# Kernel optimization log

Hardware: AMD Instinct MI355X
Metric: run time of the kernel (lower is better)

Reference implementation:

```python
import jax, jax.numpy as jnp
import numpy as np

B, N, M, D = 2, 2048, 32, 128
H, DH = 8, 16
DI = H * DH            # dim_inner = 128
S = 5                  # 1 + max_degree + max_degree, max_degree = 2
DMLP = 256             # int(2.0 * dim_inner)


def _ln(x, g):  # LayerNorm(bias=False)
    mu = x.mean(-1, keepdims=True)
    var = ((x - mu) ** 2).mean(-1, keepdims=True)
    return (x - mu) / jnp.sqrt(var + 1e-5) * g


def _softclamp(t, v=50.0):
    return jnp.tanh(t / v) * v


def _gather(a, idx):  # a: [b, n, ...], idx: [b, i, j] -> [b, i, j, ...]
    return jax.vmap(lambda t, ix: jnp.take(t, ix, axis=0))(a, idx)


def setup_inputs():
    key = jax.random.key(0)
    ks = jax.random.split(key, 24)
    w = lambda k, i, o: jax.random.normal(k, (i, o), jnp.float32) / np.sqrt(i)
    return {
        'h': jax.random.normal(ks[0], (B, N, D), jnp.float32),
        't_ij': jax.random.normal(ks[1], (B, N, M, D), jnp.float32),
        'r_ij_1': jax.random.normal(ks[2], (B, N, M, 3), jnp.float32),
        'r_ij_2': jax.random.normal(ks[3], (B, N, M, 5), jnp.float32),
        'x_1': jax.random.normal(ks[4], (B, N, D, 3), jnp.float32),
        'x_2': jax.random.normal(ks[5], (B, N, D, 5), jnp.float32),
        'g_hi': jnp.ones((D,), jnp.float32),
        'g_hj': jnp.ones((D,), jnp.float32),
        'Wq': w(ks[6], D, DI),
        'Wk': w(ks[7], D, DI),
        'Wv1': w(ks[8], D, DMLP), 'bv1': jnp.zeros((DMLP,), jnp.float32),
        'Wv2': w(ks[9], DMLP, S * DI), 'bv2': jnp.zeros((S * DI,), jnp.float32),
        'Wp1': w(ks[10], D, DMLP), 'bp1': jnp.zeros((DMLP,), jnp.float32),
        'Wp2': w(ks[11], DMLP, S * DI), 'bp2': jnp.zeros((S * DI,), jnp.float32),
        'Wek': w(ks[12], D, S * DI),
        'Wev': w(ks[13], D, S * DI),
        'Wg': w(ks[14], D, H * S), 'bg': jnp.zeros((H * S,), jnp.float32),
        'Wc': w(ks[15], DI, D),
        'neighbor_indices': jax.random.randint(ks[16], (B, N, M), 0, N),
        'neighbor_mask': jnp.ones((B, N, M), bool),
    }


def reference(h, t_ij, r_ij_1, r_ij_2, x_1, x_2, g_hi, g_hj, Wq, Wk, Wv1, bv1,
              Wv2, bv2, Wp1, bp1, Wp2, bp2, Wek, Wev, Wg, bg, Wc,
              neighbor_indices, neighbor_mask):
    b, n, m = neighbor_indices.shape
    hi = _ln(h, g_hi)
    hj = _ln(h, g_hj)
    q = (hi @ Wq).reshape(b, n, H, DH).transpose(0, 2, 1, 3)               # b h i dh
    k = hj @ Wk                                                            # b n (h dh)
    v = jax.nn.silu(hj @ Wv1 + bv1) @ Wv2 + bv2                            # b n (s h dh)
    pav = jax.nn.silu(hj @ Wp1 + bp1) @ Wp2 + bp2                          # post-attn h values
    ek = jax.nn.silu(t_ij @ Wek)                                           # b i j (s h dh)
    ev = t_ij @ Wev
    # neighbor gathers over the node axis
    k_g = _gather(k, neighbor_indices)                                     # b i j (h dh)
    v_g = _gather(v, neighbor_indices)                                     # b i j (s h dh)
    pav_g = _gather(pav, neighbor_indices)
    heads4 = lambda t: t.reshape(b, n, m, H, DH).transpose(0, 3, 1, 2, 4)          # b h i j dh
    heads5 = lambda t: t.reshape(b, n, m, S, H, DH).transpose(0, 4, 1, 2, 3, 5)    # b h i j s dh
    keys = heads4(k_g)[..., None, :] * heads5(ek)                          # edge-fused keys
    sim = _softclamp(jnp.einsum('bhid,bhijsd->bhijs', q, keys))
    sim = jnp.where(neighbor_mask[:, None, :, :, None], sim, -jnp.finfo(sim.dtype).max)
    attn = jax.nn.softmax(sim, axis=-2)                                    # softmax over neighbors j
    sea = attn[..., None] * heads5(v_g) + heads5(ev) * heads5(pav_g)       # b h i j s dh
    gates = jax.nn.sigmoid(hi @ Wg + bg).reshape(b, n, H, S)               # layout (h s)
    sea = sea * gates.transpose(0, 2, 1, 3)[:, :, :, None, :, None]        # b h i 1 s 1
    out = sea.transpose(0, 2, 3, 4, 1, 5).reshape(b, n, m, S, DI) @ Wc     # b i j s d
    h_res = out[..., 0, :].sum(axis=2)                                     # sum over neighbors
    x_res = []
    for li, (r_l, x_l) in enumerate(((r_ij_1, x_1), (r_ij_2, x_2))):
        r_part = jnp.einsum('bijm,bijd->bidm', r_l, out[..., 1 + li, :])
        xg = _gather(x_l, neighbor_indices)                                # b i j d ml
        x_res.append(r_part + jnp.einsum('bijdm,bijd->bidm', xg, out[..., 3 + li, :]))
    return (h_res, x_res[0], x_res[1])
```

## Files before the change

### kernel.cpp

```cpp
#include <hip/hip_runtime.h>
#include <hip/hip_bf16.h>
#include <cstdint>


typedef __bf16 bf16x8 __attribute__((ext_vector_type(8)));
typedef float  f32x4  __attribute__((ext_vector_type(4)));
typedef unsigned short u16;
typedef unsigned int   u32;

__device__ __forceinline__ float sigm_(float x){ return 1.f/(1.f+__expf(-x)); }
__device__ __forceinline__ float silu_(float x){ return x/(1.f+__expf(-x)); }
__device__ __forceinline__ u16 f2b(float f){
    union{float f; u32 u;} x; x.f = f;
    u32 r = x.u + 0x7FFFu + ((x.u>>16)&1u);
    return (u16)(r>>16);
}
__device__ __forceinline__ float b2f(u16 b){
    union{u32 u; float f;} x; x.u = ((u32)b)<<16; return x.f;
}
union VecU { uint4 u; bf16x8 v; u16 s[8]; };
union Vec4 { uint2 u; u16 s[4]; };
__device__ __forceinline__ bf16x8 ld8(const u16* p){ VecU x; x.u = *(const uint4*)p; return x.v; }

__global__ __launch_bounds__(256) void prep_kernel(
    const float* __restrict__ Wek, const float* __restrict__ Wev,
    const float* __restrict__ Wc,
    const float* __restrict__ x1, const float* __restrict__ x2,
    u16* __restrict__ wekT, u16* __restrict__ wevT, u16* __restrict__ wcT,
    float* __restrict__ xT1, float* __restrict__ xT2, int do_xt)
{
    const int idx = blockIdx.x*256 + threadIdx.x;
    if (idx < 81920) {
        const int n = idx >> 7, k = idx & 127;
        wekT[idx] = f2b(Wek[k*640 + n]);
        wevT[idx] = f2b(Wev[k*640 + n]);
    }
    if (idx < 16384) {
        const int d = idx >> 7, c = idx & 127;
        wcT[idx] = f2b(Wc[c*128 + d]);
    }
    if (do_xt) {
        if (idx < 4096*384) {
            const int node = idx/384, rem = idx%384, m = rem>>7, d = rem&127;
            xT1[idx] = x1[((size_t)node*128 + d)*3 + m];
        }
        if (idx < 4096*640) {
            const int node = idx/640, rem = idx%640, m = rem>>7, d = rem&127;
            xT2[idx] = x2[((size_t)node*128 + d)*5 + m];
        }
    }
}

__global__ __launch_bounds__(256) void node_kernel(
    const float* __restrict__ h,
    const float* __restrict__ g_hi, const float* __restrict__ g_hj,
    const float* __restrict__ Wq, const float* __restrict__ Wk,
    const float* __restrict__ Wv1, const float* __restrict__ bv1,
    const float* __restrict__ Wv2, const float* __restrict__ bv2,
    const float* __restrict__ Wp1, const float* __restrict__ bp1,
    const float* __restrict__ Wp2, const float* __restrict__ bp2,
    const float* __restrict__ Wg, const float* __restrict__ bg,
    float* __restrict__ qws, float* __restrict__ kws,
    float* __restrict__ vws, float* __restrict__ pavws, float* __restrict__ gws)
{
    const int tid  = threadIdx.x;
    const int base = blockIdx.x * 8;
    __shared__ __align__(16) float hi_s[8][128];
    __shared__ __align__(16) float hj_s[8][128];
    __shared__ __align__(16) float u_s[8][256];

    {
        const int wv = tid >> 6, lane = tid & 63;
        for (int r = wv; r < 8; r += 4) {
            const int node = base + r;
            float a  = h[node*128 + lane];
            float b2 = h[node*128 + 64 + lane];
            float s = a + b2;
            #pragma unroll
            for (int off = 32; off > 0; off >>= 1) s += __shfl_down(s, off);
            s = __shfl(s, 0);
            const float mu = s * (1.f/128.f);
            const float da = a - mu, db = b2 - mu;
            float v = da*da + db*db;
            #pragma unroll
            for (int off = 32; off > 0; off >>= 1) v += __shfl_down(v, off);
            v = __shfl(v, 0);
            const float rstd = rsqrtf(v*(1.f/128.f) + 1e-5f);
            hi_s[r][lane]    = da*rstd*g_hi[lane];
            hi_s[r][64+lane] = db*rstd*g_hi[64+lane];
            hj_s[r][lane]    = da*rstd*g_hj[lane];
            hj_s[r][64+lane] = db*rstd*g_hj[64+lane];
        }
    }
    __syncthreads();

    {
        const int o  = tid & 127;
        const int r0 = (tid >> 7) * 4;
        float aq[4], ak[4];
        #pragma unroll
        for (int r=0;r<4;r++){ aq[r]=0.f; ak[r]=0.f; }
        for (int c0=0;c0<128;c0+=4) {
            float wq0=Wq[(c0+0)*128+o], wq1=Wq[(c0+1)*128+o], wq2=Wq[(c0+2)*128+o], wq3=Wq[(c0+3)*128+o];
            float wk0=Wk[(c0+0)*128+o], wk1=Wk[(c0+1)*128+o], wk2=Wk[(c0+2)*128+o], wk3=Wk[(c0+3)*128+o];
            #pragma unroll
            for (int r=0;r<4;r++) {
                float4 hi4 = *(const float4*)(&hi_s[r0+r][c0]);
                float4 hj4 = *(const float4*)(&hj_s[r0+r][c0]);
                aq[r] += hi4.x*wq0; aq[r] += hi4.y*wq1; aq[r] += hi4.z*wq2; aq[r] += hi4.w*wq3;
                ak[r] += hj4.x*wk0; ak[r] += hj4.y*wk1; ak[r] += hj4.z*wk2; ak[r] += hj4.w*wk3;
            }
        }
        #pragma unroll
        for (int r=0;r<4;r++) {
            qws[(size_t)(base+r0+r)*128 + o] = aq[r];
            kws[(size_t)(base+r0+r)*128 + o] = ak[r];
        }
    }

    {
        const int o = tid;
        float acc[8];
        const float bias = bv1[o];
        #pragma unroll
        for (int r=0;r<8;r++) acc[r]=bias;
        for (int c0=0;c0<128;c0+=4) {
            float w0=Wv1[(c0+0)*256+o], w1=Wv1[(c0+1)*256+o], w2=Wv1[(c0+2)*256+o], w3=Wv1[(c0+3)*256+o];
            #pragma unroll
            for (int r=0;r<8;r++) {
                float4 u4 = *(const float4*)(&hj_s[r][c0]);
                acc[r] += u4.x*w0; acc[r] += u4.y*w1; acc[r] += u4.z*w2; acc[r] += u4.w*w3;
            }
        }
        #pragma unroll
        for (int r=0;r<8;r++) u_s[r][o] = silu_(acc[r]);
    }
    __syncthreads();

    for (int o=tid; o<640; o+=256) {
        float acc[8];
        const float bias = bv2[o];
        #pragma unroll
        for (int r=0;r<8;r++) acc[r]=bias;
        for (int c0=0;c0<256;c0+=4) {
            float w0=Wv2[(c0+0)*640+o], w1=Wv2[(c0+1)*640+o], w2=Wv2[(c0+2)*640+o], w3=Wv2[(c0+3)*640+o];
            #pragma unroll
            for (int r=0;r<8;r++) {
                float4 u4 = *(const float4*)(&u_s[r][c0]);
                acc[r] += u4.x*w0; acc[r] += u4.y*w1; acc[r] += u4.z*w2; acc[r] += u4.w*w3;
            }
        }
        #pragma unroll
        for (int r=0;r<8;r++) vws[(size_t)(base+r)*640 + o] = acc[r];
    }
    __syncthreads();

    {
        const int o = tid;
        float acc[8];
        const float bias = bp1[o];
        #pragma unroll
        for (int r=0;r<8;r++) acc[r]=bias;
        for (int c0=0;c0<128;c0+=4) {
            float w0=Wp1[(c0+0)*256+o], w1=Wp1[(c0+1)*256+o], w2=Wp1[(c0+2)*256+o], w3=Wp1[(c0+3)*256+o];
            #pragma unroll
            for (int r=0;r<8;r++) {
                float4 u4 = *(const float4*)(&hj_s[r][c0]);
                acc[r] += u4.x*w0; acc[r] += u4.y*w1; acc[r] += u4.z*w2; acc[r] += u4.w*w3;
            }
        }
        #pragma unroll
        for (int r=0;r<8;r++) u_s[r][o] = silu_(acc[r]);
    }
    __syncthreads();

    for (int o=tid; o<640; o+=256) {
        float acc[8];
        const float bias = bp2[o];
        #pragma unroll
        for (int r=0;r<8;r++) acc[r]=bias;
        for (int c0=0;c0<256;c0+=4) {
            float w0=Wp2[(c0+0)*640+o], w1=Wp2[(c0+1)*640+o], w2=Wp2[(c0+2)*640+o], w3=Wp2[(c0+3)*640+o];
            #pragma unroll
            for (int r=0;r<8;r++) {
                float4 u4 = *(const float4*)(&u_s[r][c0]);
                acc[r] += u4.x*w0; acc[r] += u4.y*w1; acc[r] += u4.z*w2; acc[r] += u4.w*w3;
            }
        }
        #pragma unroll
        for (int r=0;r<8;r++) pavws[(size_t)(base+r)*640 + o] = acc[r];
    }

    for (int idx=tid; idx<8*40; idx+=256) {
        const int r = idx/40, hs = idx%40;
        float s = bg[hs];
        for (int c=0;c<128;c++) s += hi_s[r][c]*Wg[c*40+hs];
        gws[(size_t)(base+r)*40 + hs] = sigm_(s);
    }
}

template<bool XT>
__global__ __launch_bounds__(512,4) void edge_kernel(
    const float* __restrict__ t_ij,
    const float* __restrict__ r1, const float* __restrict__ r2,
    const float* __restrict__ x1, const float* __restrict__ x2,
    const float* __restrict__ xT1, const float* __restrict__ xT2,
    const u16* __restrict__ wekT, const u16* __restrict__ wevT,
    const u16* __restrict__ wcT,
    const int* __restrict__ nidx,
    const float* __restrict__ qws, const float* __restrict__ kws,
    const float* __restrict__ vws, const float* __restrict__ pavws,
    const float* __restrict__ gws,
    float* __restrict__ out)
{
    const int node = blockIdx.x;
    const int bN   = (node >> 11) << 11;
    const int tid  = threadIdx.x;
    const int grp  = tid >> 8;
    const int ltid = tid & 255;
    const int lane = ltid & 63, w = ltid >> 6;
    const int ll   = lane & 15, lh = lane >> 4;

    __shared__ __align__(16) u16   tj_s[32*128];
    __shared__ __align__(16) u16   chunk_s[2][80*128];
    __shared__ float sim_s[32][40];
    __shared__ __align__(16) float q_s[128];
    __shared__ float g_s[40];
    __shared__ int   jn_s[32];

    u16* chunk = chunk_s[grp];

    if (tid < 32) jn_s[tid] = nidx[node*32 + tid];
    else if (tid >= 64 && tid < 192) q_s[tid-64] = qws[(size_t)node*128 + (tid-64)];
    else if (tid >= 192 && tid < 232) g_s[tid-192] = gws[(size_t)node*40 + (tid-192)];
    __syncthreads();

    bf16x8 wcf[2][4];
    #pragma unroll
    for (int dlt=0;dlt<2;dlt++)
        #pragma unroll
        for (int ks=0;ks<4;ks++)
            wcf[dlt][ks] = ld8(wcT + (size_t)((w*2+dlt)*16 + ll)*128 + ks*32 + lh*8);

    float kq[16];
    if (ltid < 128) {
        const int j = grp*16 + (ltid >> 3), c0 = (ltid & 7) * 16;
        const float* tp = t_ij + (size_t)node*4096 + j*128 + c0;
        float4 t0 = *(const float4*)(tp+0);
        float4 t1 = *(const float4*)(tp+4);
        float4 t2 = *(const float4*)(tp+8);
        float4 t3 = *(const float4*)(tp+12);
        VecU p0, p1;
        p0.s[0]=f2b(t0.x); p0.s[1]=f2b(t0.y); p0.s[2]=f2b(t0.z); p0.s[3]=f2b(t0.w);
        p0.s[4]=f2b(t1.x); p0.s[5]=f2b(t1.y); p0.s[6]=f2b(t1.z); p0.s[7]=f2b(t1.w);
        p1.s[0]=f2b(t2.x); p1.s[1]=f2b(t2.y); p1.s[2]=f2b(t2.z); p1.s[3]=f2b(t2.w);
        p1.s[4]=f2b(t3.x); p1.s[5]=f2b(t3.y); p1.s[6]=f2b(t3.z); p1.s[7]=f2b(t3.w);
        const int el = (j*128 + c0) ^ ((j&7)<<3);
        *(uint4*)(tj_s + el)       = p0.u;
        *(uint4*)(tj_s + (el ^ 8)) = p1.u;

        const float* kp = kws + ((size_t)(bN + jn_s[j]))*128 + c0;
        #pragma unroll
        for (int i=0;i<16;i+=4) {
            float4 kv = *(const float4*)(kp+i);
            float4 qv = *(const float4*)(&q_s[c0+i]);
            kq[i+0] = qv.x*kv.x; kq[i+1] = qv.y*kv.y;
            kq[i+2] = qv.z*kv.z; kq[i+3] = qv.w*kv.w;
        }
    }
    __syncthreads();

    bf16x8 tfr[4];
    #pragma unroll
    for (int ks=0;ks<4;ks++) {
        const int j = grp*16 + ll;
        tfr[ks] = ld8(tj_s + ((j*128 + ks*32 + lh*8) ^ ((j&7)<<3)));
    }
    #pragma unroll 2
    for (int t=0;t<10;t++) {
        const int nt = w + 4*t;
        const u16* wp = wekT + (size_t)(nt*16 + ll)*128 + lh*8;
        __builtin_amdgcn_s_setprio(1);
        f32x4 aA = {0.f,0.f,0.f,0.f}, aB = {0.f,0.f,0.f,0.f};
        aA = __builtin_amdgcn_mfma_f32_16x16x32_bf16(ld8(wp +  0), tfr[0], aA, 0,0,0);
        aB = __builtin_amdgcn_mfma_f32_16x16x32_bf16(ld8(wp + 32), tfr[1], aB, 0,0,0);
        aA = __builtin_amdgcn_mfma_f32_16x16x32_bf16(ld8(wp + 64), tfr[2], aA, 0,0,0);
        aB = __builtin_amdgcn_mfma_f32_16x16x32_bf16(ld8(wp + 96), tfr[3], aB, 0,0,0);
        __builtin_amdgcn_s_setprio(0);
        f32x4 acc = aA + aB;
        const int ss = nt >> 3, c0 = (nt&7)*16 + lh*4;
        const int r  = ss*16 + ll;
        Vec4 pk;
        #pragma unroll
        for (int reg=0;reg<4;reg++) pk.s[reg] = f2b(silu_(acc[reg]));
        *(uint2*)(chunk + ((r*128 + c0) ^ ((r&7)<<3))) = pk.u;
    }
    __syncthreads();

    if (ltid < 128) {
        const int jj = ltid >> 3, hh = ltid & 7;
        #pragma unroll
        for (int ss=0; ss<5; ss++) {
            const int r = ss*16 + jj;
            const int el = (r*128 + hh*16) ^ ((r&7)<<3);
            VecU e0, e1;
            e0.u = *(const uint4*)(chunk + el);
            e1.u = *(const uint4*)(chunk + (el^8));
            float s = 0.f;
            #pragma unroll
            for (int i=0;i<8;i++) s += kq[i]   * b2f(e0.s[i]);
            #pragma unroll
            for (int i=0;i<8;i++) s += kq[8+i] * b2f(e1.s[i]);
            sim_s[grp*16 + jj][hh*5 + ss] = 50.f * tanhf(s*0.02f);
        }
    }
    __syncthreads();

    if (tid < 40) {
        float mx = -1e30f;
        #pragma unroll
        for (int j=0;j<32;j++) mx = fmaxf(mx, sim_s[j][tid]);
        float sum = 0.f;
        #pragma unroll
        for (int j=0;j<32;j++) sum += __expf(sim_s[j][tid]-mx);
        const float inv = 1.f/sum;
        #pragma unroll
        for (int j=0;j<32;j++) sim_s[j][tid] = __expf(sim_s[j][tid]-mx)*inv;
    }
    __syncthreads();

    float accH[2] = {0,0};
    float aR1[3][2], aX1[3][2], aR2[5][2], aX2[5][2];
    #pragma unroll
    for (int m=0;m<3;m++){ aR1[m][0]=aR1[m][1]=0.f; aX1[m][0]=aX1[m][1]=0.f; }
    #pragma unroll
    for (int m=0;m<5;m++){ aR2[m][0]=aR2[m][1]=0.f; aX2[m][0]=aX2[m][1]=0.f; }

    {
        const int edge = grp*16 + ll;
        const int nj   = jn_s[edge];
        const float* vrow = vws   + (size_t)(bN + nj)*640;
        const float* prow = pavws + (size_t)(bN + nj)*640;

        float4 v4c = *(const float4*)(vrow + (w*16 + lh*4));
        float4 pvc = *(const float4*)(prow + (w*16 + lh*4));
        #pragma unroll 2
        for (int t=0;t<10;t++) {
            const int nt = w + 4*t;
            const float4 v4 = v4c, pv = pvc;
            if (t < 9) {
                const int o0n = (nt+4)*16 + lh*4;
                v4c = *(const float4*)(vrow + o0n);
                pvc = *(const float4*)(prow + o0n);
            }
            const u16* wp = wevT + (size_t)(nt*16 + ll)*128 + lh*8;
            __builtin_amdgcn_s_setprio(1);
            f32x4 aA = {0.f,0.f,0.f,0.f}, aB = {0.f,0.f,0.f,0.f};
            aA = __builtin_amdgcn_mfma_f32_16x16x32_bf16(ld8(wp +  0), tfr[0], aA, 0,0,0);
            aB = __builtin_amdgcn_mfma_f32_16x16x32_bf16(ld8(wp + 32), tfr[1], aB, 0,0,0);
            aA = __builtin_amdgcn_mfma_f32_16x16x32_bf16(ld8(wp + 64), tfr[2], aA, 0,0,0);
            aB = __builtin_amdgcn_mfma_f32_16x16x32_bf16(ld8(wp + 96), tfr[3], aB, 0,0,0);
            __builtin_amdgcn_s_setprio(0);
            f32x4 acc = aA + aB;
            const int ss = nt >> 3, hsu = (nt&7)*5 + ss;
            const int c0 = (nt&7)*16 + lh*4;
            const float gate = g_s[hsu];
            const float attn = sim_s[edge][hsu];
            Vec4 w4;
            w4.s[0] = f2b((attn*v4.x + acc[0]*pv.x)*gate);
            w4.s[1] = f2b((attn*v4.y + acc[1]*pv.y)*gate);
            w4.s[2] = f2b((attn*v4.z + acc[2]*pv.z)*gate);
            w4.s[3] = f2b((attn*v4.w + acc[3]*pv.w)*gate);
            const int r = ss*16 + ll;
            *(uint2*)(chunk + ((r*128 + c0) ^ ((r&7)<<3))) = w4.u;
        }
    }
    __syncthreads();

    #pragma unroll 1
    for (int mt=0; mt<5; ++mt) {
        bf16x8 afr[4];
        #pragma unroll
        for (int ks=0;ks<4;ks++) {
            const int r = mt*16 + ll;
            afr[ks] = ld8(chunk + ((r*128 + ks*32 + lh*8) ^ ((r&7)<<3)));
        }
        #pragma unroll
        for (int dlt=0; dlt<2; ++dlt) {
            __builtin_amdgcn_s_setprio(1);
            f32x4 dA = {0.f,0.f,0.f,0.f}, dB = {0.f,0.f,0.f,0.f};
            dA = __builtin_amdgcn_mfma_f32_16x16x32_bf16(afr[0], wcf[dlt][0], dA, 0,0,0);
            dB = __builtin_amdgcn_mfma_f32_16x16x32_bf16(afr[1], wcf[dlt][1], dB, 0,0,0);
            dA = __builtin_amdgcn_mfma_f32_16x16x32_bf16(afr[2], wcf[dlt][2], dA, 0,0,0);
            dB = __builtin_amdgcn_mfma_f32_16x16x32_bf16(afr[3], wcf[dlt][3], dB, 0,0,0);
            __builtin_amdgcn_s_setprio(0);
            f32x4 dacc = dA + dB;
            const int d = (w*2+dlt)*16 + ll;
            if (mt == 0) {
                accH[dlt] += dacc[0]+dacc[1]+dacc[2]+dacc[3];
            } else if (mt == 1) {
                #pragma unroll
                for (int reg=0;reg<4;reg++) {
                    const int j = grp*16 + lh*4 + reg;
                    const float* rp = r1 + ((size_t)node*32 + j)*3;
                    const float p = dacc[reg];
                    #pragma unroll
                    for (int m=0;m<3;m++) aR1[m][dlt] += rp[m]*p;
                }
            } else if (mt == 2) {
                #pragma unroll
                for (int reg=0;reg<4;reg++) {
                    const int j = grp*16 + lh*4 + reg;
                    const float* rp = r2 + ((size_t)node*32 + j)*5;
                    const float p = dacc[reg];
                    #pragma unroll
                    for (int m=0;m<5;m++) aR2[m][dlt] += rp[m]*p;
                }
            } else if (mt == 3) {
                #pragma unroll
                for (int reg=0;reg<4;reg++) {
                    const int j = grp*16 + lh*4 + reg;
                    const int njg = jn_s[j];
                    const float p = dacc[reg];
                    if (XT) {
                        const float* xp = xT1 + ((size_t)(bN + njg)*3)*128 + d;
                        #pragma unroll
                        for (int m=0;m<3;m++) aX1[m][dlt] += xp[m*128]*p;
                    } else {
                        const float* xp = x1 + ((size_t)(bN + njg)*128 + d)*3;
                        #pragma unroll
                        for (int m=0;m<3;m++) aX1[m][dlt] += xp[m]*p;
                    }
                }
            } else {
                #pragma unroll
                for (int reg=0;reg<4;reg++) {
                    const int j = grp*16 + lh*4 + reg;
                    const int njg = jn_s[j];
                    const float p = dacc[reg];
                    if (XT) {
                        const float* xp = xT2 + ((size_t)(bN + njg)*5)*128 + d;
                        #pragma unroll
                        for (int m=0;m<5;m++) aX2[m][dlt] += xp[m*128]*p;
                    } else {
                        const float* xp = x2 + ((size_t)(bN + njg)*128 + d)*5;
                        #pragma unroll
                        for (int m=0;m<5;m++) aX2[m][dlt] += xp[m]*p;
                    }
                }
            }
        }
    }

    #define RED2(x) { x += __shfl_xor(x,16); x += __shfl_xor(x,32); }
    #pragma unroll
    for (int dlt=0; dlt<2; ++dlt) {
        RED2(accH[dlt]);
        #pragma unroll
        for (int m=0;m<3;m++){ RED2(aR1[m][dlt]); RED2(aX1[m][dlt]); }
        #pragma unroll
        for (int m=0;m<5;m++){ RED2(aR2[m][dlt]); RED2(aX2[m][dlt]); }
    }
    __syncthreads();

    float* xch = (float*)chunk_s[0];
    if (grp == 1 && lh == 0) {
        #pragma unroll
        for (int dlt=0; dlt<2; ++dlt) {
            const int d = (w*2+dlt)*16 + ll;
            float* p = xch + d*17;
            p[0] = accH[dlt];
            #pragma unroll
            for (int m=0;m<3;m++){ p[1+m] = aR1[m][dlt]; p[4+m] = aX1[m][dlt]; }
            #pragma unroll
            for (int m=0;m<5;m++){ p[7+m] = aR2[m][dlt]; p[12+m] = aX2[m][dlt]; }
        }
    }
    __syncthreads();
    if (grp == 0 && lh == 0) {
        #pragma unroll
        for (int dlt=0; dlt<2; ++dlt) {
            const int d = (w*2+dlt)*16 + ll;
            const float* p = xch + d*17;
            out[(size_t)node*128 + d] = accH[dlt] + p[0];
            float* o1 = out + 524288 + ((size_t)node*128 + d)*3;
            #pragma unroll
            for (int m=0;m<3;m++) o1[m] = (aR1[m][dlt] + p[1+m]) + (aX1[m][dlt] + p[4+m]);
            float* o2 = out + 2097152 + ((size_t)node*128 + d)*5;
            #pragma unroll
            for (int m=0;m<5;m++) o2[m] = (aR2[m][dlt] + p[7+m]) + (aX2[m][dlt] + p[12+m]);
        }
    }
}

extern "C" void kernel_launch(void* const* d_in, const int* in_sizes, int n_in,
                              void* d_out, int out_size, void* d_ws, size_t ws_size,
                              hipStream_t stream)
{
    const float* h    = (const float*)d_in[0];
    const float* t_ij = (const float*)d_in[1];
    const float* r1   = (const float*)d_in[2];
    const float* r2   = (const float*)d_in[3];
    const float* x1   = (const float*)d_in[4];
    const float* x2   = (const float*)d_in[5];
    const float* g_hi = (const float*)d_in[6];
    const float* g_hj = (const float*)d_in[7];
    const float* Wq   = (const float*)d_in[8];
    const float* Wk   = (const float*)d_in[9];
    const float* Wv1  = (const float*)d_in[10];
    const float* bv1  = (const float*)d_in[11];
    const float* Wv2  = (const float*)d_in[12];
    const float* bv2  = (const float*)d_in[13];
    const float* Wp1  = (const float*)d_in[14];
    const float* bp1  = (const float*)d_in[15];
    const float* Wp2  = (const float*)d_in[16];
    const float* bp2  = (const float*)d_in[17];
    const float* Wek  = (const float*)d_in[18];
    const float* Wev  = (const float*)d_in[19];
    const float* Wg   = (const float*)d_in[20];
    const float* bg   = (const float*)d_in[21];
    const float* Wc   = (const float*)d_in[22];
    const int*   nidx = (const int*)d_in[23];

    char* ws = (char*)d_ws;
    float* qws   = (float*)ws;  ws += (size_t)4096*128*4;
    float* kws   = (float*)ws;  ws += (size_t)4096*128*4;
    float* gws   = (float*)ws;  ws += (size_t)4096*40*4;
    float* vws   = (float*)ws;  ws += (size_t)4096*640*4;
    float* pavws = (float*)ws;  ws += (size_t)4096*640*4;
    u16*   wekT  = (u16*)ws;    ws += (size_t)81920*2;
    u16*   wevT  = (u16*)ws;    ws += (size_t)81920*2;
    u16*   wcT   = (u16*)ws;    ws += (size_t)16384*2;
    float* xT1   = (float*)ws;  ws += (size_t)4096*384*4;
    float* xT2   = (float*)ws;  ws += (size_t)4096*640*4;
    const size_t need_xt = (size_t)(ws - (char*)d_ws);
    const int use_xt = (ws_size >= need_xt) ? 1 : 0;

    hipLaunchKernelGGL(prep_kernel, dim3(use_xt ? 10240 : 320), dim3(256), 0, stream,
        Wek, Wev, Wc, x1, x2, wekT, wevT, wcT, xT1, xT2, use_xt);

    hipLaunchKernelGGL(node_kernel, dim3(512), dim3(256), 0, stream,
        h, g_hi, g_hj, Wq, Wk, Wv1, bv1, Wv2, bv2, Wp1, bp1, Wp2, bp2, Wg, bg,
        qws, kws, vws, pavws, gws);

    if (use_xt) {
        hipLaunchKernelGGL(edge_kernel<true>, dim3(4096), dim3(512), 0, stream,
            t_ij, r1, r2, x1, x2, xT1, xT2, wekT, wevT, wcT, nidx,
            qws, kws, vws, pavws, gws, (float*)d_out);
    } else {
        hipLaunchKernelGGL(edge_kernel<false>, dim3(4096), dim3(512), 0, stream,
            t_ij, r1, r2, x1, x2, xT1, xT2, wekT, wevT, wcT, nidx,
            qws, kws, vws, pavws, gws, (float*)d_out);
    }
}
```

Measured before the change: 596.6 us.

## Interleave v/pav rows, double-buffer gather loop, hoist x gathers before MFMA

The node kernel now writes v and pav into one interleaved buffer, with each 4-wide chunk of v followed by the matching 4 of pav. The edge kernel can then fetch both from one contiguous 32-byte region per neighbor. The value-building loop is restructured to process two tiles per iteration with register prefetch of the next pair. The gathered x_1/x_2 neighbor values are loaded into registers once per output column block, before the Wc MFMA loop instead of inside it, so the memory latency overlaps with the matrix work. This raises register pressure, which could hurt occupancy at 512 threads x 4 blocks.

```diff
diff --git a/kernel.cpp b/kernel.cpp
--- a/kernel.cpp
+++ b/kernel.cpp
@@ -61,7 +61,7 @@
     const float* __restrict__ Wp2, const float* __restrict__ bp2,
     const float* __restrict__ Wg, const float* __restrict__ bg,
     float* __restrict__ qws, float* __restrict__ kws,
-    float* __restrict__ vws, float* __restrict__ pavws, float* __restrict__ gws)
+    float* __restrict__ vpws, float* __restrict__ gws)
 {
     const int tid  = threadIdx.x;
     const int base = blockIdx.x * 8;
@@ -151,7 +151,8 @@
             }
         }
         #pragma unroll
-        for (int r=0;r<8;r++) vws[(size_t)(base+r)*640 + o] = acc[r];
+        for (int r=0;r<8;r++)
+            vpws[(size_t)(base+r)*1280 + (o>>2)*8 + (o&3)] = acc[r];
     }
     __syncthreads();
 
@@ -188,7 +189,8 @@
             }
         }
         #pragma unroll
-        for (int r=0;r<8;r++) pavws[(size_t)(base+r)*640 + o] = acc[r];
+        for (int r=0;r<8;r++)
+            vpws[(size_t)(base+r)*1280 + (o>>2)*8 + 4 + (o&3)] = acc[r];
     }
 
     for (int idx=tid; idx<8*40; idx+=256) {
@@ -209,7 +211,7 @@
     const u16* __restrict__ wcT,
     const int* __restrict__ nidx,
     const float* __restrict__ qws, const float* __restrict__ kws,
-    const float* __restrict__ vws, const float* __restrict__ pavws,
+    const float* __restrict__ vpws,
     const float* __restrict__ gws,
     float* __restrict__ out)
 {
@@ -329,30 +331,12 @@
     }
     __syncthreads();
 
-    float accH[2] = {0,0};
-    float aR1[3][2], aX1[3][2], aR2[5][2], aX2[5][2];
-    #pragma unroll
-    for (int m=0;m<3;m++){ aR1[m][0]=aR1[m][1]=0.f; aX1[m][0]=aX1[m][1]=0.f; }
-    #pragma unroll
-    for (int m=0;m<5;m++){ aR2[m][0]=aR2[m][1]=0.f; aX2[m][0]=aX2[m][1]=0.f; }
-
+    const int edge = grp*16 + ll;
     {
-        const int edge = grp*16 + ll;
         const int nj   = jn_s[edge];
-        const float* vrow = vws   + (size_t)(bN + nj)*640;
-        const float* prow = pavws + (size_t)(bN + nj)*640;
-
-        float4 v4c = *(const float4*)(vrow + (w*16 + lh*4));
-        float4 pvc = *(const float4*)(prow + (w*16 + lh*4));
-        #pragma unroll 2
-        for (int t=0;t<10;t++) {
-            const int nt = w + 4*t;
-            const float4 v4 = v4c, pv = pvc;
-            if (t < 9) {
-                const int o0n = (nt+4)*16 + lh*4;
-                v4c = *(const float4*)(vrow + o0n);
-                pvc = *(const float4*)(prow + o0n);
-            }
+        const float* vprow = vpws + (size_t)(bN + nj)*1280;
+
+        auto body = [&](int nt, const float4& v4, const float4& pv) {
             const u16* wp = wevT + (size_t)(nt*16 + ll)*128 + lh*8;
             __builtin_amdgcn_s_setprio(1);
             f32x4 aA = {0.f,0.f,0.f,0.f}, aB = {0.f,0.f,0.f,0.f};
@@ -373,20 +357,67 @@
             w4.s[3] = f2b((attn*v4.w + acc[3]*pv.w)*gate);
             const int r = ss*16 + ll;
             *(uint2*)(chunk + ((r*128 + c0) ^ ((r&7)<<3))) = w4.u;
-        }
-    }
-    __syncthreads();
-
-    #pragma unroll 1
-    for (int mt=0; mt<5; ++mt) {
-        bf16x8 afr[4];
-        #pragma unroll
-        for (int ks=0;ks<4;ks++) {
-            const int r = mt*16 + ll;
-            afr[ks] = ld8(chunk + ((r*128 + ks*32 + lh*8) ^ ((r&7)<<3)));
-        }
-        #pragma unroll
-        for (int dlt=0; dlt<2; ++dlt) {
+        };
+
+        int qa = (w+0)*4 + lh, qb = (w+4)*4 + lh;
+        float4 va = *(const float4*)(vprow + qa*8);
+        float4 pa = *(const float4*)(vprow + qa*8 + 4);
+        float4 vb = *(const float4*)(vprow + qb*8);
+        float4 pb = *(const float4*)(vprow + qb*8 + 4);
+        for (int tt=0; tt<5; ++tt) {
+            const int nt0 = w + 8*tt, nt1 = nt0 + 4;
+            const float4 v0 = va, p0 = pa, v1 = vb, p1 = pb;
+            if (tt < 4) {
+                const int qa2 = (nt0+8)*4 + lh, qb2 = (nt1+8)*4 + lh;
+                va = *(const float4*)(vprow + qa2*8);
+                pa = *(const float4*)(vprow + qa2*8 + 4);
+                vb = *(const float4*)(vprow + qb2*8);
+                pb = *(const float4*)(vprow + qb2*8 + 4);
+            }
+            body(nt0, v0, p0);
+            body(nt1, v1, p1);
+        }
+    }
+    __syncthreads();
+
+    float accH[2] = {0,0};
+    float aR1[3][2], aX1[3][2], aR2[5][2], aX2[5][2];
+    #pragma unroll
+    for (int m=0;m<3;m++){ aR1[m][0]=aR1[m][1]=0.f; aX1[m][0]=aX1[m][1]=0.f; }
+    #pragma unroll
+    for (int m=0;m<5;m++){ aR2[m][0]=aR2[m][1]=0.f; aX2[m][0]=aX2[m][1]=0.f; }
+
+    #pragma unroll
+    for (int dlt=0; dlt<2; ++dlt) {
+        const int d = (w*2+dlt)*16 + ll;
+        float xh1[4][3], xh2[4][5];
+        #pragma unroll
+        for (int reg=0;reg<4;reg++) {
+            const int njg = jn_s[grp*16 + lh*4 + reg];
+            if (XT) {
+                const float* p1 = xT1 + ((size_t)(bN + njg)*3)*128 + d;
+                const float* p2 = xT2 + ((size_t)(bN + njg)*5)*128 + d;
+                #pragma unroll
+                for (int m=0;m<3;m++) xh1[reg][m] = p1[m*128];
+                #pragma unroll
+                for (int m=0;m<5;m++) xh2[reg][m] = p2[m*128];
+            } else {
+                const float* p1 = x1 + ((size_t)(bN + njg)*128 + d)*3;
+                const float* p2 = x2 + ((size_t)(bN + njg)*128 + d)*5;
+                #pragma unroll
+                for (int m=0;m<3;m++) xh1[reg][m] = p1[m];
+                #pragma unroll
+                for (int m=0;m<5;m++) xh2[reg][m] = p2[m];
+            }
+        }
+        #pragma unroll 1
+        for (int mt=0; mt<5; ++mt) {
+            bf16x8 afr[4];
+            #pragma unroll
+            for (int ks=0;ks<4;ks++) {
+                const int r = mt*16 + ll;
+                afr[ks] = ld8(chunk + ((r*128 + ks*32 + lh*8) ^ ((r&7)<<3)));
+            }
             __builtin_amdgcn_s_setprio(1);
             f32x4 dA = {0.f,0.f,0.f,0.f}, dB = {0.f,0.f,0.f,0.f};
             dA = __builtin_amdgcn_mfma_f32_16x16x32_bf16(afr[0], wcf[dlt][0], dA, 0,0,0);
@@ -395,7 +426,6 @@
             dB = __builtin_amdgcn_mfma_f32_16x16x32_bf16(afr[3], wcf[dlt][3], dB, 0,0,0);
             __builtin_amdgcn_s_setprio(0);
             f32x4 dacc = dA + dB;
-            const int d = (w*2+dlt)*16 + ll;
             if (mt == 0) {
                 accH[dlt] += dacc[0]+dacc[1]+dacc[2]+dacc[3];
             } else if (mt == 1) {
@@ -419,34 +449,16 @@
             } else if (mt == 3) {
                 #pragma unroll
                 for (int reg=0;reg<4;reg++) {
-                    const int j = grp*16 + lh*4 + reg;
-                    const int njg = jn_s[j];
                     const float p = dacc[reg];
-                    if (XT) {
-                        const float* xp = xT1 + ((size_t)(bN + njg)*3)*128 + d;
-                        #pragma unroll
-                        for (int m=0;m<3;m++) aX1[m][dlt] += xp[m*128]*p;
-                    } else {
-                        const float* xp = x1 + ((size_t)(bN + njg)*128 + d)*3;
-                        #pragma unroll
-                        for (int m=0;m<3;m++) aX1[m][dlt] += xp[m]*p;
-                    }
+                    #pragma unroll
+                    for (int m=0;m<3;m++) aX1[m][dlt] += xh1[reg][m]*p;
                 }
             } else {
                 #pragma unroll
                 for (int reg=0;reg<4;reg++) {
-                    const int j = grp*16 + lh*4 + reg;
-                    const int njg = jn_s[j];
                     const float p = dacc[reg];
-                    if (XT) {
-                        const float* xp = xT2 + ((size_t)(bN + njg)*5)*128 + d;
-                        #pragma unroll
-                        for (int m=0;m<5;m++) aX2[m][dlt] += xp[m*128]*p;
-                    } else {
-                        const float* xp = x2 + ((size_t)(bN + njg)*128 + d)*5;
-                        #pragma unroll
-                        for (int m=0;m<5;m++) aX2[m][dlt] += xp[m]*p;
-                    }
+                    #pragma unroll
+                    for (int m=0;m<5;m++) aX2[m][dlt] += xh2[reg][m]*p;
                 }
             }
         }
@@ -526,8 +538,7 @@
     float* qws   = (float*)ws;  ws += (size_t)4096*128*4;
     float* kws   = (float*)ws;  ws += (size_t)4096*128*4;
     float* gws   = (float*)ws;  ws += (size_t)4096*40*4;
-    float* vws   = (float*)ws;  ws += (size_t)4096*640*4;
-    float* pavws = (float*)ws;  ws += (size_t)4096*640*4;
+    float* vpws  = (float*)ws;  ws += (size_t)4096*1280*4;
     u16*   wekT  = (u16*)ws;    ws += (size_t)81920*2;
     u16*   wevT  = (u16*)ws;    ws += (size_t)81920*2;
     u16*   wcT   = (u16*)ws;    ws += (size_t)16384*2;
@@ -541,15 +552,15 @@
 
     hipLaunchKernelGGL(node_kernel, dim3(512), dim3(256), 0, stream,
         h, g_hi, g_hj, Wq, Wk, Wv1, bv1, Wv2, bv2, Wp1, bp1, Wp2, bp2, Wg, bg,
-        qws, kws, vws, pavws, gws);
+        qws, kws, vpws, gws);
 
     if (use_xt) {
         hipLaunchKernelGGL(edge_kernel<true>, dim3(4096), dim3(512), 0, stream,
             t_ij, r1, r2, x1, x2, xT1, xT2, wekT, wevT, wcT, nidx,
-            qws, kws, vws, pavws, gws, (float*)d_out);
+            qws, kws, vpws, gws, (float*)d_out);
     } else {
         hipLaunchKernelGGL(edge_kernel<false>, dim3(4096), dim3(512), 0, stream,
             t_ij, r1, r2, x1, x2, xT1, xT2, wekT, wevT, wcT, nidx,
-            qws, kws, vws, pavws, gws, (float*)d_out);
+            qws, kws, vpws, gws, (float*)d_out);
     }
 }
```

After: 592.6 us. Within noise of the previous version (-0.7%).
